# Kernel optimization log

Hardware: AMD Instinct MI355X
Metric: run time of the kernel (lower is better)

## Reference

```python
import jax, jax.numpy as jnp
import numpy as np

NEG_SLOPE = 0.2  # keras 'leaky_relu' default negative slope

def _leaky_relu(t):
    return jnp.where(t >= 0, t, NEG_SLOPE * t)

def setup_inputs() -> dict:
    key = jax.random.key(0)
    kx, kq, kk, kv, ko, kg = jax.random.split(key, 6)
    B, H, W, C, A = 4, 64, 64, 256, 128
    x = jax.random.normal(kx, (B, H, W, C), dtype=jnp.float32)
    # 1x1 conv kernels == [Cin, Cout] matrices; glorot-normal-ish scaling
    Wq = jax.random.normal(kq, (C, A), dtype=jnp.float32) * (2.0 / (C + A)) ** 0.5
    Wk = jax.random.normal(kk, (C, A), dtype=jnp.float32) * (2.0 / (C + A)) ** 0.5
    Wv = jax.random.normal(kv, (C, A), dtype=jnp.float32) * (2.0 / (C + A)) ** 0.5
    Wo = jax.random.normal(ko, (A, C), dtype=jnp.float32) * (2.0 / (A + C)) ** 0.5
    # ChannelLearnableMultiplier weight: truncated_normal(0, 0.01) ~ small values near 0
    w_gamma = jax.random.normal(kg, (1, 1, 1, C), dtype=jnp.float32) * 0.01
    return {"x": x, "Wq": Wq, "Wk": Wk, "Wv": Wv, "Wo": Wo, "w_gamma": w_gamma}

def reference(x, Wq, Wk, Wv, Wo, w_gamma):
    B, H, W, C = x.shape
    A = Wq.shape[1]
    # 1x1 conv projections with leaky_relu activation, flatten spatial -> [B, N, A]
    q = _leaky_relu(jnp.einsum('bhwc,ca->bhwa', x, Wq)).reshape(B, H * W, A)
    k = _leaky_relu(jnp.einsum('bhwc,ca->bhwa', x, Wk)).reshape(B, H * W, A)
    v = _leaky_relu(jnp.einsum('bhwc,ca->bhwa', x, Wv)).reshape(B, H * W, A)
    # keras Attention(use_scale=False, score_mode='dot'): softmax(q k^T) v
    scores = jnp.einsum('bnd,bmd->bnm', q, k)          # [B, N, N]
    attn = jax.nn.softmax(scores, axis=-1)
    o = jnp.einsum('bnm,bmd->bnd', attn, v)            # [B, N, A]
    o = o.reshape(B, H, W, A)
    # output 1x1 conv, linear activation
    y = jnp.einsum('bhwa,ac->bhwc', o, Wo)
    # ChannelLearnableMultiplier: tanh(relu(1 + w)) * y
    return jnp.tanh(jax.nn.relu(1.0 + w_gamma)) * y
```

## Files before the change

### kernel.cpp

```cpp
#include <hip/hip_runtime.h>
#include <hip/hip_bf16.h>
#include <cstdint>
#include <cstddef>

typedef __bf16 bf16x8 __attribute__((ext_vector_type(8)));
typedef _Float16 f16x8 __attribute__((ext_vector_type(8)));
typedef short short8 __attribute__((ext_vector_type(8)));
typedef short short4v __attribute__((ext_vector_type(4)));
typedef float f32x4 __attribute__((ext_vector_type(4)));

__device__ __forceinline__ unsigned short f2bf(float f) {
    union { float f; uint32_t u; } v; v.f = f;
    uint32_t u = v.u;
    return (unsigned short)((u + 0x7FFFu + ((u >> 16) & 1u)) >> 16);
}
__device__ __forceinline__ float bf2f(unsigned short h) {
    union { uint32_t u; float f; } v; v.u = ((uint32_t)h) << 16;
    return v.f;
}
__device__ __forceinline__ unsigned short f2h(float f) {
    union { _Float16 h; unsigned short u; } v; v.h = (_Float16)f;
    return v.u;
}

__global__ __launch_bounds__(256) void prep_kernel(
    const float* __restrict__ Wq, const float* __restrict__ Wk,
    const float* __restrict__ Wv, const float* __restrict__ Wo,
    unsigned short* __restrict__ wt_hi,
    unsigned short* __restrict__ wt_lo,
    unsigned short* __restrict__ wot)
{
    const int bid = blockIdx.x, t = threadIdx.x;
    __shared__ __align__(16) unsigned short Th[128][72], Tl[128][72];
    __shared__ __align__(16) unsigned short T[64][136];
    if (bid < 12) {
        const int proj = bid >> 2, kc = bid & 3;
        const float* W = (proj == 0) ? Wq : ((proj == 1) ? Wk : Wv);
        for (int r = 0; r < 32; ++r) {
            int idx = r * 256 + t;
            int kk = idx >> 7, n = idx & 127;
            float w = W[(size_t)(kc * 64 + kk) * 128 + n];
            unsigned short h = f2bf(w);
            Th[n][kk] = h;
            Tl[n][kk] = f2bf(w - bf2f(h));
        }
        __syncthreads();
        int n = t >> 1, k0 = (t & 1) * 32;
        size_t off = (size_t)proj * 32768 + (size_t)kc * 8192 + (size_t)n * 64 + k0;
        #pragma unroll
        for (int j = 0; j < 4; ++j) {
            *(short8*)(wt_hi + off + j * 8) = *(const short8*)(&Th[n][k0 + j * 8]);
            *(short8*)(wt_lo + off + j * 8) = *(const short8*)(&Tl[n][k0 + j * 8]);
        }
    } else if (bid < 16) {
        const int c0 = (bid - 12) * 64;
        for (int r = 0; r < 32; ++r) {
            int idx = r * 256 + t;
            int a = idx >> 6, cc = idx & 63;
            T[cc][a] = f2bf(Wo[(size_t)a * 256 + c0 + cc]);
        }
        __syncthreads();
        int cc = t >> 2, a0 = (t & 3) * 32;
        #pragma unroll
        for (int j = 0; j < 4; ++j)
            *(short8*)(wot + (size_t)(c0 + cc) * 128 + a0 + j * 8) =
                *(const short8*)(&T[cc][a0 + j * 8]);
    }
}

__global__ __launch_bounds__(256) void qkv_kernel(
    const float* __restrict__ x,
    const unsigned short* __restrict__ wt_hi,
    const unsigned short* __restrict__ wt_lo,
    unsigned short* __restrict__ qkv_ws)
{
    const int rowtile = blockIdx.x;
    const int proj    = blockIdx.y;
    unsigned short* outqk = qkv_ws + (size_t)proj * 2097152u;
    unsigned short* vt    = qkv_ws + (size_t)2 * 2097152u;
    const bool need_lo = (proj < 2);

    const int tid  = threadIdx.x;
    const int lane = tid & 63, wave = tid >> 6;
    const int lo   = lane & 15, quad = lane >> 4;

    __shared__ __align__(16) unsigned short Xh[64][72], Xl[64][72];
    __shared__ __align__(16) unsigned short Wh[128][72], Wl[128][72];

    f32x4 acc[8];
    #pragma unroll
    for (int i = 0; i < 8; ++i) acc[i] = (f32x4){0.f, 0.f, 0.f, 0.f};

    const int wn = tid >> 1, wk0 = (tid & 1) * 32;

    for (int kc = 0; kc < 4; ++kc) {
        __syncthreads();
        #pragma unroll
        for (int i = 0; i < 4; ++i) {
            int flat4 = (i * 256 + tid) * 4;
            int row = flat4 >> 6, col = flat4 & 63;
            float4 tv4 = *(const float4*)(x + (size_t)(rowtile * 64 + row) * 256 + kc * 64 + col);
            float tv[4] = {tv4.x, tv4.y, tv4.z, tv4.w};
            short4v h, l;
            #pragma unroll
            for (int j = 0; j < 4; ++j) {
                unsigned short hj = f2bf(tv[j]);
                h[j] = (short)hj;
                l[j] = (short)f2bf(tv[j] - bf2f(hj));
            }
            *(short4v*)(&Xh[row][col]) = h;
            if (need_lo) *(short4v*)(&Xl[row][col]) = l;
        }
        {
            const size_t off = (size_t)proj * 32768 + (size_t)kc * 8192 + (size_t)wn * 64 + wk0;
            #pragma unroll
            for (int j = 0; j < 4; ++j)
                *(short8*)(&Wh[wn][wk0 + j * 8]) = *(const short8*)(wt_hi + off + j * 8);
            if (need_lo) {
                #pragma unroll
                for (int j = 0; j < 4; ++j)
                    *(short8*)(&Wl[wn][wk0 + j * 8]) = *(const short8*)(wt_lo + off + j * 8);
            }
        }
        __syncthreads();
        #pragma unroll
        for (int ks = 0; ks < 2; ++ks) {
            bf16x8 ah = *(const bf16x8*)(&Xh[wave * 16 + lo][ks * 32 + quad * 8]);
            #pragma unroll
            for (int nb = 0; nb < 8; ++nb) {
                bf16x8 bh = *(const bf16x8*)(&Wh[nb * 16 + lo][ks * 32 + quad * 8]);
                acc[nb] = __builtin_amdgcn_mfma_f32_16x16x32_bf16(ah, bh, acc[nb], 0, 0, 0);
                if (need_lo) {
                    bf16x8 al = *(const bf16x8*)(&Xl[wave * 16 + lo][ks * 32 + quad * 8]);
                    bf16x8 bl = *(const bf16x8*)(&Wl[nb * 16 + lo][ks * 32 + quad * 8]);
                    acc[nb] = __builtin_amdgcn_mfma_f32_16x16x32_bf16(al, bh, acc[nb], 0, 0, 0);
                    acc[nb] = __builtin_amdgcn_mfma_f32_16x16x32_bf16(ah, bl, acc[nb], 0, 0, 0);
                }
            }
        }
    }
    if (proj < 2) {
        #pragma unroll
        for (int nb = 0; nb < 8; ++nb) {
            #pragma unroll
            for (int r = 0; r < 4; ++r) {
                float v = acc[nb][r];
                v = (v >= 0.f) ? v : 0.2f * v;
                int m = rowtile * 64 + wave * 16 + quad * 4 + r;
                outqk[(size_t)m * 128 + nb * 16 + lo] = f2h(v);
            }
        }
    } else {
        const int b  = rowtile >> 6;
        const int sb = (rowtile & 63) * 64;
        #pragma unroll
        for (int nb = 0; nb < 8; ++nb) {
            #pragma unroll
            for (int r = 0; r < 4; ++r) {
                float v = acc[nb][r];
                v = (v >= 0.f) ? v : 0.2f * v;
                int seq = sb + wave * 16 + quad * 4 + r;
                int d   = nb * 16 + lo;
                vt[(size_t)b * 524288 + (size_t)d * 4096 + seq] = f2bf(v);
            }
        }
    }
}

__global__ __launch_bounds__(256) void attn_kernel(
    const unsigned short* __restrict__ qkv_ws,
    unsigned short* __restrict__ part,
    float* __restrict__ lpart,
    int chunk)
{
    const int b  = blockIdx.x;
    const int qt = blockIdx.y;
    const int z  = blockIdx.z;
    const int tid  = threadIdx.x;
    const int lane = tid & 63, wave = tid >> 6;
    const int lo   = lane & 15, quad = lane >> 4;

    const unsigned short* q  = qkv_ws;
    const unsigned short* k  = qkv_ws + 2097152u;
    const unsigned short* vt = qkv_ws + (size_t)2 * 2097152u + (size_t)b * 524288u;

    __shared__ __align__(16) unsigned short Ks[32][136];
    __shared__ __align__(16) unsigned short Vt[128][40];
    __shared__ __align__(16) unsigned short Ps[4][32][40];

    const int qbase = qt * 128 + wave * 32;
    f16x8 qf[2][4];
    #pragma unroll
    for (int g = 0; g < 2; ++g)
        #pragma unroll
        for (int ks = 0; ks < 4; ++ks)
            qf[g][ks] = *(const f16x8*)(q + ((size_t)(b * 4096 + qbase + g * 16 + lo)) * 128
                                          + ks * 32 + quad * 8);

    f32x4 oacc[2][8];
    #pragma unroll
    for (int g = 0; g < 2; ++g)
        #pragma unroll
        for (int i = 0; i < 8; ++i) oacc[g][i] = (f32x4){0.f, 0.f, 0.f, 0.f};
    float lsum[2][4];
    #pragma unroll
    for (int g = 0; g < 2; ++g)
        #pragma unroll
        for (int r = 0; r < 4; ++r) lsum[g][r] = 1e-30f;

    const float LOG2E  = 1.44269504088896f;
    const float NSHIFT = -40.0f * 1.44269504088896f;

    const int c0 = tid, c1 = 256 + tid;
    const int krow0 = c0 >> 4, kcol0 = (c0 & 15) * 8;
    const int krow1 = (c1 - 256) >> 4 + 0;
    const int vd0 = c0 >> 2, vs0 = (c0 & 3) * 8;
    const int vd1 = (c1 - 256) >> 2, vs1 = ((c1 - 256) & 3) * 8;
    const int krow1b = 16 + (tid >> 4), kcol1b = (tid & 15) * 8;
    const int vd1b = 64 + (tid >> 2), vs1b = (tid & 3) * 8;
    (void)krow1; (void)vd1; (void)vs1; (void)c1;

    const int niter = chunk >> 5;
    const int sbase = z * chunk;

    short8 ka, kb, va, vb;
    {
        ka = *(const short8*)(k + ((size_t)(b * 4096 + sbase + krow0)) * 128 + kcol0);
        kb = *(const short8*)(k + ((size_t)(b * 4096 + sbase + krow1b)) * 128 + kcol1b);
        va = *(const short8*)(vt + (size_t)vd0 * 4096 + sbase + vs0);
        vb = *(const short8*)(vt + (size_t)vd1b * 4096 + sbase + vs1b);
    }

    for (int kt = 0; kt < niter; ++kt) {
        __syncthreads();
        *(short8*)(&Ks[krow0][kcol0]) = ka;
        *(short8*)(&Ks[krow1b][kcol1b]) = kb;
        *(short8*)(&Vt[vd0][vs0]) = va;
        *(short8*)(&Vt[vd1b][vs1b]) = vb;
        __syncthreads();
        if (kt + 1 < niter) {
            const int s1 = sbase + (kt + 1) * 32;
            ka = *(const short8*)(k + ((size_t)(b * 4096 + s1 + krow0)) * 128 + kcol0);
            kb = *(const short8*)(k + ((size_t)(b * 4096 + s1 + krow1b)) * 128 + kcol1b);
            va = *(const short8*)(vt + (size_t)vd0 * 4096 + s1 + vs0);
            vb = *(const short8*)(vt + (size_t)vd1b * 4096 + s1 + vs1b);
        }

        f32x4 s[2][2];
        s[0][0] = (f32x4){0.f,0.f,0.f,0.f}; s[0][1] = (f32x4){0.f,0.f,0.f,0.f};
        s[1][0] = (f32x4){0.f,0.f,0.f,0.f}; s[1][1] = (f32x4){0.f,0.f,0.f,0.f};
        #pragma unroll
        for (int ks = 0; ks < 4; ++ks) {
            #pragma unroll
            for (int nb = 0; nb < 2; ++nb) {
                f16x8 bf = *(const f16x8*)(&Ks[nb * 16 + lo][ks * 32 + quad * 8]);
                s[0][nb] = __builtin_amdgcn_mfma_f32_16x16x32_f16(qf[0][ks], bf, s[0][nb], 0, 0, 0);
                s[1][nb] = __builtin_amdgcn_mfma_f32_16x16x32_f16(qf[1][ks], bf, s[1][nb], 0, 0, 0);
            }
        }
        #pragma unroll
        for (int g = 0; g < 2; ++g) {
            #pragma unroll
            for (int nb = 0; nb < 2; ++nb) {
                #pragma unroll
                for (int r = 0; r < 4; ++r) {
                    float t = fminf(fmaf(s[g][nb][r], LOG2E, NSHIFT), 125.0f);
                    union { float f; uint32_t u; } pv; pv.f = exp2f(t);
                    unsigned short pt = (unsigned short)(pv.u >> 16);
                    lsum[g][r] += bf2f(pt);
                    Ps[wave][g * 16 + quad * 4 + r][nb * 16 + lo] = pt;
                }
            }
        }
        bf16x8 pf0 = *(const bf16x8*)(&Ps[wave][lo][quad * 8]);
        bf16x8 pf1 = *(const bf16x8*)(&Ps[wave][16 + lo][quad * 8]);
        #pragma unroll
        for (int nb = 0; nb < 8; ++nb) {
            bf16x8 vf = *(const bf16x8*)(&Vt[nb * 16 + lo][quad * 8]);
            oacc[0][nb] = __builtin_amdgcn_mfma_f32_16x16x32_bf16(pf0, vf, oacc[0][nb], 0, 0, 0);
            oacc[1][nb] = __builtin_amdgcn_mfma_f32_16x16x32_bf16(pf1, vf, oacc[1][nb], 0, 0, 0);
        }
    }

    #pragma unroll
    for (int g = 0; g < 2; ++g) {
        #pragma unroll
        for (int r = 0; r < 4; ++r) {
            float xr = lsum[g][r];
            #pragma unroll
            for (int m = 1; m < 16; m <<= 1) xr += __shfl_xor(xr, m, 64);
            lsum[g][r] = xr;
        }
        #pragma unroll
        for (int nb = 0; nb < 8; ++nb) {
            #pragma unroll
            for (int r = 0; r < 4; ++r) {
                int m = b * 4096 + qbase + g * 16 + quad * 4 + r;
                part[((size_t)z * 16384 + m) * 128 + nb * 16 + lo] = f2bf(oacc[g][nb][r]);
            }
        }
        if (lo == 0) {
            #pragma unroll
            for (int r = 0; r < 4; ++r) {
                int m = b * 4096 + qbase + g * 16 + quad * 4 + r;
                lpart[(size_t)z * 16384 + m] = lsum[g][r];
            }
        }
    }
}

__global__ __launch_bounds__(256) void outproj_kernel(
    const unsigned short* __restrict__ part,
    const float* __restrict__ lpart,
    const unsigned short* __restrict__ wot,
    const float* __restrict__ wg,
    float* __restrict__ out,
    int nsplit)
{
    const int rowtile = blockIdx.x;
    const int ch      = blockIdx.y;
    const int tid  = threadIdx.x;
    const int lane = tid & 63, wave = tid >> 6;
    const int lo   = lane & 15, quad = lane >> 4;

    __shared__ __align__(16) unsigned short Os[64][136];
    __shared__ __align__(16) unsigned short WoT[128][136];

    #pragma unroll
    for (int i = 0; i < 4; ++i) {
        int flat = (i * 256 + tid) * 8;
        int row = flat >> 7, col = flat & 127;
        int m = rowtile * 64 + row;
        float acc8[8] = {0.f,0.f,0.f,0.f,0.f,0.f,0.f,0.f};
        float l = 0.f;
        for (int zz = 0; zz < nsplit; ++zz) {
            short8 t = *(const short8*)(part + ((size_t)zz * 16384 + m) * 128 + col);
            #pragma unroll
            for (int j = 0; j < 8; ++j) acc8[j] += bf2f((unsigned short)t[j]);
            l += lpart[(size_t)zz * 16384 + m];
        }
        float inv = 1.0f / l;
        short8 o8;
        #pragma unroll
        for (int j = 0; j < 8; ++j) o8[j] = (short)f2bf(acc8[j] * inv);
        *(short8*)(&Os[row][col]) = o8;
    }
    {
        int c = tid >> 1, a0 = (tid & 1) * 64;
        #pragma unroll
        for (int j = 0; j < 8; ++j)
            *(short8*)(&WoT[c][a0 + j * 8]) =
                *(const short8*)(wot + (size_t)(ch * 128 + c) * 128 + a0 + j * 8);
    }
    __syncthreads();

    f32x4 acc[8];
    #pragma unroll
    for (int i = 0; i < 8; ++i) acc[i] = (f32x4){0.f, 0.f, 0.f, 0.f};
    #pragma unroll
    for (int ks = 0; ks < 4; ++ks) {
        bf16x8 a = *(const bf16x8*)(&Os[wave * 16 + lo][ks * 32 + quad * 8]);
        #pragma unroll
        for (int nb = 0; nb < 8; ++nb) {
            bf16x8 bf = *(const bf16x8*)(&WoT[nb * 16 + lo][ks * 32 + quad * 8]);
            acc[nb] = __builtin_amdgcn_mfma_f32_16x16x32_bf16(a, bf, acc[nb], 0, 0, 0);
        }
    }
    #pragma unroll
    for (int nb = 0; nb < 8; ++nb) {
        int c = ch * 128 + nb * 16 + lo;
        float g = 1.0f + wg[c];
        if (g < 0.f) g = 0.f;
        g = tanhf(g);
        #pragma unroll
        for (int r = 0; r < 4; ++r) {
            int m = rowtile * 64 + wave * 16 + quad * 4 + r;
            out[(size_t)m * 256 + c] = acc[nb][r] * g;
        }
    }
}

extern "C" void kernel_launch(void* const* d_in, const int* in_sizes, int n_in,
                              void* d_out, int out_size, void* d_ws, size_t ws_size,
                              hipStream_t stream) {
    const float* x  = (const float*)d_in[0];
    const float* Wq = (const float*)d_in[1];
    const float* Wk = (const float*)d_in[2];
    const float* Wv = (const float*)d_in[3];
    const float* Wo = (const float*)d_in[4];
    const float* wg = (const float*)d_in[5];
    float* out = (float*)d_out;

    unsigned short* ws = (unsigned short*)d_ws;
    const int nsplit = (ws_size >= (size_t)47000000) ? 8 : 4;
    const int chunk = 4096 / nsplit;

    unsigned short* qkv_ws = ws;
    unsigned short* part   = ws + (size_t)3 * 2097152u;
    unsigned short* wt_hi  = part;
    unsigned short* wt_lo  = part + 98304u;
    float* lpart = (float*)(part + (size_t)nsplit * 2097152u);
    unsigned short* wot = (unsigned short*)(lpart + (size_t)nsplit * 16384u);

    prep_kernel<<<dim3(16), 256, 0, stream>>>(Wq, Wk, Wv, Wo, wt_hi, wt_lo, wot);
    qkv_kernel<<<dim3(256, 3), 256, 0, stream>>>(x, wt_hi, wt_lo, qkv_ws);
    attn_kernel<<<dim3(4, 32, nsplit), 256, 0, stream>>>(qkv_ws, part, lpart, chunk);
    outproj_kernel<<<dim3(256, 2), 256, 0, stream>>>(part, lpart, wot, wg, out, nsplit);
}
```

Baseline: 178.6 us.

## Precompute x bf16 hi/lo split once and merge outproj channel halves per block

Moves the fp32-to-bf16 hi/lo split of x into the prep kernel, so qkv blocks load ready-made bf16 tiles instead of converting x three times (once per projection). Also precomputes the gamma multiplier once, and has each outproj block loop over both channel halves, so the split-K partial reduction is done once instead of twice. The extra x staging pass adds global traffic and a serial dependency, and outproj now launches half as many blocks.

```diff
diff --git a/kernel.cpp b/kernel.cpp
--- a/kernel.cpp
+++ b/kernel.cpp
@@ -26,13 +26,17 @@
 __global__ __launch_bounds__(256) void prep_kernel(
     const float* __restrict__ Wq, const float* __restrict__ Wk,
     const float* __restrict__ Wv, const float* __restrict__ Wo,
+    const float* __restrict__ wg, const float* __restrict__ x,
     unsigned short* __restrict__ wt_hi,
     unsigned short* __restrict__ wt_lo,
-    unsigned short* __restrict__ wot)
+    unsigned short* __restrict__ wot,
+    float* __restrict__ gamma,
+    unsigned short* __restrict__ xh,
+    unsigned short* __restrict__ xl,
+    int use_pre)
 {
     const int bid = blockIdx.x, t = threadIdx.x;
     __shared__ __align__(16) unsigned short Th[128][72], Tl[128][72];
-    __shared__ __align__(16) unsigned short T[64][136];
     if (bid < 12) {
         const int proj = bid >> 2, kc = bid & 3;
         const float* W = (proj == 0) ? Wq : ((proj == 1) ? Wk : Wv);
@@ -54,25 +58,50 @@
         }
     } else if (bid < 16) {
         const int c0 = (bid - 12) * 64;
+        unsigned short* T = &Th[0][0];
         for (int r = 0; r < 32; ++r) {
             int idx = r * 256 + t;
             int a = idx >> 6, cc = idx & 63;
-            T[cc][a] = f2bf(Wo[(size_t)a * 256 + c0 + cc]);
+            T[cc * 136 + a] = f2bf(Wo[(size_t)a * 256 + c0 + cc]);
         }
         __syncthreads();
         int cc = t >> 2, a0 = (t & 3) * 32;
         #pragma unroll
         for (int j = 0; j < 4; ++j)
             *(short8*)(wot + (size_t)(c0 + cc) * 128 + a0 + j * 8) =
-                *(const short8*)(&T[cc][a0 + j * 8]);
+                *(const short8*)(&T[cc * 136 + a0 + j * 8]);
+    } else if (bid == 16) {
+        float g = 1.0f + wg[t];
+        if (g < 0.f) g = 0.f;
+        gamma[t] = tanhf(g);
+    } else if (use_pre) {
+        const int bx = bid - 17;
+        #pragma unroll 4
+        for (int it = 0; it < 32; ++it) {
+            size_t ci = (size_t)bx * 8192 + it * 256 + t;
+            float4 tv4 = *(const float4*)(x + ci * 4);
+            float tv[4] = {tv4.x, tv4.y, tv4.z, tv4.w};
+            short4v h, l;
+            #pragma unroll
+            for (int j = 0; j < 4; ++j) {
+                unsigned short hj = f2bf(tv[j]);
+                h[j] = (short)hj;
+                l[j] = (short)f2bf(tv[j] - bf2f(hj));
+            }
+            *(short4v*)(xh + ci * 4) = h;
+            *(short4v*)(xl + ci * 4) = l;
+        }
     }
 }
 
 __global__ __launch_bounds__(256) void qkv_kernel(
     const float* __restrict__ x,
+    const unsigned short* __restrict__ xh,
+    const unsigned short* __restrict__ xl,
     const unsigned short* __restrict__ wt_hi,
     const unsigned short* __restrict__ wt_lo,
-    unsigned short* __restrict__ qkv_ws)
+    unsigned short* __restrict__ qkv_ws,
+    int use_pre)
 {
     const int rowtile = blockIdx.x;
     const int proj    = blockIdx.y;
@@ -95,21 +124,32 @@
 
     for (int kc = 0; kc < 4; ++kc) {
         __syncthreads();
-        #pragma unroll
-        for (int i = 0; i < 4; ++i) {
-            int flat4 = (i * 256 + tid) * 4;
-            int row = flat4 >> 6, col = flat4 & 63;
-            float4 tv4 = *(const float4*)(x + (size_t)(rowtile * 64 + row) * 256 + kc * 64 + col);
-            float tv[4] = {tv4.x, tv4.y, tv4.z, tv4.w};
-            short4v h, l;
-            #pragma unroll
-            for (int j = 0; j < 4; ++j) {
-                unsigned short hj = f2bf(tv[j]);
-                h[j] = (short)hj;
-                l[j] = (short)f2bf(tv[j] - bf2f(hj));
-            }
-            *(short4v*)(&Xh[row][col]) = h;
-            if (need_lo) *(short4v*)(&Xl[row][col]) = l;
+        if (use_pre) {
+            #pragma unroll
+            for (int j = 0; j < 2; ++j) {
+                int ci = tid * 2 + j;
+                int row = ci >> 3, col = (ci & 7) * 8;
+                size_t g = (size_t)(rowtile * 64 + row) * 256 + kc * 64 + col;
+                *(short8*)(&Xh[row][col]) = *(const short8*)(xh + g);
+                if (need_lo) *(short8*)(&Xl[row][col]) = *(const short8*)(xl + g);
+            }
+        } else {
+            #pragma unroll
+            for (int i = 0; i < 4; ++i) {
+                int flat4 = (i * 256 + tid) * 4;
+                int row = flat4 >> 6, col = flat4 & 63;
+                float4 tv4 = *(const float4*)(x + (size_t)(rowtile * 64 + row) * 256 + kc * 64 + col);
+                float tv[4] = {tv4.x, tv4.y, tv4.z, tv4.w};
+                short4v h, l;
+                #pragma unroll
+                for (int j = 0; j < 4; ++j) {
+                    unsigned short hj = f2bf(tv[j]);
+                    h[j] = (short)hj;
+                    l[j] = (short)f2bf(tv[j] - bf2f(hj));
+                }
+                *(short4v*)(&Xh[row][col]) = h;
+                if (need_lo) *(short4v*)(&Xl[row][col]) = l;
+            }
         }
         {
             const size_t off = (size_t)proj * 32768 + (size_t)kc * 8192 + (size_t)wn * 64 + wk0;
@@ -211,39 +251,33 @@
     const float LOG2E  = 1.44269504088896f;
     const float NSHIFT = -40.0f * 1.44269504088896f;
 
-    const int c0 = tid, c1 = 256 + tid;
-    const int krow0 = c0 >> 4, kcol0 = (c0 & 15) * 8;
-    const int krow1 = (c1 - 256) >> 4 + 0;
-    const int vd0 = c0 >> 2, vs0 = (c0 & 3) * 8;
-    const int vd1 = (c1 - 256) >> 2, vs1 = ((c1 - 256) & 3) * 8;
-    const int krow1b = 16 + (tid >> 4), kcol1b = (tid & 15) * 8;
-    const int vd1b = 64 + (tid >> 2), vs1b = (tid & 3) * 8;
-    (void)krow1; (void)vd1; (void)vs1; (void)c1;
+    const int krow0 = tid >> 4,        kcol0 = (tid & 15) * 8;
+    const int krow1 = 16 + (tid >> 4), kcol1 = (tid & 15) * 8;
+    const int vd0 = tid >> 2,          vs0 = (tid & 3) * 8;
+    const int vd1 = 64 + (tid >> 2),   vs1 = (tid & 3) * 8;
 
     const int niter = chunk >> 5;
     const int sbase = z * chunk;
 
     short8 ka, kb, va, vb;
-    {
-        ka = *(const short8*)(k + ((size_t)(b * 4096 + sbase + krow0)) * 128 + kcol0);
-        kb = *(const short8*)(k + ((size_t)(b * 4096 + sbase + krow1b)) * 128 + kcol1b);
-        va = *(const short8*)(vt + (size_t)vd0 * 4096 + sbase + vs0);
-        vb = *(const short8*)(vt + (size_t)vd1b * 4096 + sbase + vs1b);
-    }
+    ka = *(const short8*)(k + ((size_t)(b * 4096 + sbase + krow0)) * 128 + kcol0);
+    kb = *(const short8*)(k + ((size_t)(b * 4096 + sbase + krow1)) * 128 + kcol1);
+    va = *(const short8*)(vt + (size_t)vd0 * 4096 + sbase + vs0);
+    vb = *(const short8*)(vt + (size_t)vd1 * 4096 + sbase + vs1);
 
     for (int kt = 0; kt < niter; ++kt) {
         __syncthreads();
         *(short8*)(&Ks[krow0][kcol0]) = ka;
-        *(short8*)(&Ks[krow1b][kcol1b]) = kb;
+        *(short8*)(&Ks[krow1][kcol1]) = kb;
         *(short8*)(&Vt[vd0][vs0]) = va;
-        *(short8*)(&Vt[vd1b][vs1b]) = vb;
+        *(short8*)(&Vt[vd1][vs1]) = vb;
         __syncthreads();
         if (kt + 1 < niter) {
             const int s1 = sbase + (kt + 1) * 32;
             ka = *(const short8*)(k + ((size_t)(b * 4096 + s1 + krow0)) * 128 + kcol0);
-            kb = *(const short8*)(k + ((size_t)(b * 4096 + s1 + krow1b)) * 128 + kcol1b);
+            kb = *(const short8*)(k + ((size_t)(b * 4096 + s1 + krow1)) * 128 + kcol1);
             va = *(const short8*)(vt + (size_t)vd0 * 4096 + s1 + vs0);
-            vb = *(const short8*)(vt + (size_t)vd1b * 4096 + s1 + vs1b);
+            vb = *(const short8*)(vt + (size_t)vd1 * 4096 + s1 + vs1);
         }
 
         f32x4 s[2][2];
@@ -313,12 +347,11 @@
     const unsigned short* __restrict__ part,
     const float* __restrict__ lpart,
     const unsigned short* __restrict__ wot,
-    const float* __restrict__ wg,
+    const float* __restrict__ gamma,
     float* __restrict__ out,
     int nsplit)
 {
     const int rowtile = blockIdx.x;
-    const int ch      = blockIdx.y;
     const int tid  = threadIdx.x;
     const int lane = tid & 63, wave = tid >> 6;
     const int lo   = lane & 15, quad = lane >> 4;
@@ -345,37 +378,37 @@
         for (int j = 0; j < 8; ++j) o8[j] = (short)f2bf(acc8[j] * inv);
         *(short8*)(&Os[row][col]) = o8;
     }
-    {
-        int c = tid >> 1, a0 = (tid & 1) * 64;
+
+    const int wc = tid >> 1, wa0 = (tid & 1) * 64;
+    for (int ch = 0; ch < 2; ++ch) {
+        if (ch) __syncthreads();
         #pragma unroll
         for (int j = 0; j < 8; ++j)
-            *(short8*)(&WoT[c][a0 + j * 8]) =
-                *(const short8*)(wot + (size_t)(ch * 128 + c) * 128 + a0 + j * 8);
-    }
-    __syncthreads();
-
-    f32x4 acc[8];
-    #pragma unroll
-    for (int i = 0; i < 8; ++i) acc[i] = (f32x4){0.f, 0.f, 0.f, 0.f};
-    #pragma unroll
-    for (int ks = 0; ks < 4; ++ks) {
-        bf16x8 a = *(const bf16x8*)(&Os[wave * 16 + lo][ks * 32 + quad * 8]);
+            *(short8*)(&WoT[wc][wa0 + j * 8]) =
+                *(const short8*)(wot + (size_t)(ch * 128 + wc) * 128 + wa0 + j * 8);
+        __syncthreads();
+
+        f32x4 acc[8];
+        #pragma unroll
+        for (int i = 0; i < 8; ++i) acc[i] = (f32x4){0.f, 0.f, 0.f, 0.f};
+        #pragma unroll
+        for (int ks = 0; ks < 4; ++ks) {
+            bf16x8 a = *(const bf16x8*)(&Os[wave * 16 + lo][ks * 32 + quad * 8]);
+            #pragma unroll
+            for (int nb = 0; nb < 8; ++nb) {
+                bf16x8 bf = *(const bf16x8*)(&WoT[nb * 16 + lo][ks * 32 + quad * 8]);
+                acc[nb] = __builtin_amdgcn_mfma_f32_16x16x32_bf16(a, bf, acc[nb], 0, 0, 0);
+            }
+        }
         #pragma unroll
         for (int nb = 0; nb < 8; ++nb) {
-            bf16x8 bf = *(const bf16x8*)(&WoT[nb * 16 + lo][ks * 32 + quad * 8]);
-            acc[nb] = __builtin_amdgcn_mfma_f32_16x16x32_bf16(a, bf, acc[nb], 0, 0, 0);
-        }
-    }
-    #pragma unroll
-    for (int nb = 0; nb < 8; ++nb) {
-        int c = ch * 128 + nb * 16 + lo;
-        float g = 1.0f + wg[c];
-        if (g < 0.f) g = 0.f;
-        g = tanhf(g);
-        #pragma unroll
-        for (int r = 0; r < 4; ++r) {
-            int m = rowtile * 64 + wave * 16 + quad * 4 + r;
-            out[(size_t)m * 256 + c] = acc[nb][r] * g;
+            int c = ch * 128 + nb * 16 + lo;
+            float g = gamma[c];
+            #pragma unroll
+            for (int r = 0; r < 4; ++r) {
+                int m = rowtile * 64 + wave * 16 + quad * 4 + r;
+                out[(size_t)m * 256 + c] = acc[nb][r] * g;
+            }
         }
     }
 }
@@ -392,18 +425,23 @@
     float* out = (float*)d_out;
 
     unsigned short* ws = (unsigned short*)d_ws;
-    const int nsplit = (ws_size >= (size_t)47000000) ? 8 : 4;
-    const int chunk = 4096 / nsplit;
+    const int use_pre = (ws_size >= (size_t)47000000) ? 1 : 0;
+    const int nsplit  = use_pre ? 8 : 4;
+    const int chunk   = 4096 / nsplit;
 
     unsigned short* qkv_ws = ws;
     unsigned short* part   = ws + (size_t)3 * 2097152u;
     unsigned short* wt_hi  = part;
     unsigned short* wt_lo  = part + 98304u;
+    unsigned short* xh     = part + 262144u;
+    unsigned short* xl     = xh + 4194304u;
     float* lpart = (float*)(part + (size_t)nsplit * 2097152u);
     unsigned short* wot = (unsigned short*)(lpart + (size_t)nsplit * 16384u);
-
-    prep_kernel<<<dim3(16), 256, 0, stream>>>(Wq, Wk, Wv, Wo, wt_hi, wt_lo, wot);
-    qkv_kernel<<<dim3(256, 3), 256, 0, stream>>>(x, wt_hi, wt_lo, qkv_ws);
+    float* gamma = (float*)(wot + 32768u);
+
+    prep_kernel<<<dim3(use_pre ? 145 : 17), 256, 0, stream>>>(
+        Wq, Wk, Wv, Wo, wg, x, wt_hi, wt_lo, wot, gamma, xh, xl, use_pre);
+    qkv_kernel<<<dim3(256, 3), 256, 0, stream>>>(x, xh, xl, wt_hi, wt_lo, qkv_ws, use_pre);
     attn_kernel<<<dim3(4, 32, nsplit), 256, 0, stream>>>(qkv_ws, part, lpart, chunk);
-    outproj_kernel<<<dim3(256, 2), 256, 0, stream>>>(part, lpart, wot, wg, out, nsplit);
-}
+    outproj_kernel<<<dim3(256), 256, 0, stream>>>(part, lpart, wot, gamma, out, nsplit);
+}
```

After: 173.9 us. 1.03x faster.

## Double-buffer K/V tiles in attention and merge output-projection channel halves

Applied to the files above, without the earlier changes.

The attention kernel now keeps two LDS buffers for K and V tiles. The next tile is written into the idle buffer after the PV MFMAs, which removes one of the two barriers per iteration, and V is stored in a split layout so each lane reads it contiguously. The output-projection kernel loops over both channel halves inside one block, so the softmax partial combine is no longer done twice. The gamma multiplier is precomputed once in the prep kernel. In exchange, LDS use in attention goes up and the output kernel launches half as many blocks.

```diff
diff --git a/kernel.cpp b/kernel.cpp
--- a/kernel.cpp
+++ b/kernel.cpp
@@ -26,13 +26,14 @@
 __global__ __launch_bounds__(256) void prep_kernel(
     const float* __restrict__ Wq, const float* __restrict__ Wk,
     const float* __restrict__ Wv, const float* __restrict__ Wo,
+    const float* __restrict__ wg,
     unsigned short* __restrict__ wt_hi,
     unsigned short* __restrict__ wt_lo,
-    unsigned short* __restrict__ wot)
+    unsigned short* __restrict__ wot,
+    float* __restrict__ gamma)
 {
     const int bid = blockIdx.x, t = threadIdx.x;
     __shared__ __align__(16) unsigned short Th[128][72], Tl[128][72];
-    __shared__ __align__(16) unsigned short T[64][136];
     if (bid < 12) {
         const int proj = bid >> 2, kc = bid & 3;
         const float* W = (proj == 0) ? Wq : ((proj == 1) ? Wk : Wv);
@@ -54,17 +55,22 @@
         }
     } else if (bid < 16) {
         const int c0 = (bid - 12) * 64;
+        unsigned short* T = &Th[0][0];
         for (int r = 0; r < 32; ++r) {
             int idx = r * 256 + t;
             int a = idx >> 6, cc = idx & 63;
-            T[cc][a] = f2bf(Wo[(size_t)a * 256 + c0 + cc]);
+            T[cc * 136 + a] = f2bf(Wo[(size_t)a * 256 + c0 + cc]);
         }
         __syncthreads();
         int cc = t >> 2, a0 = (t & 3) * 32;
         #pragma unroll
         for (int j = 0; j < 4; ++j)
             *(short8*)(wot + (size_t)(c0 + cc) * 128 + a0 + j * 8) =
-                *(const short8*)(&T[cc][a0 + j * 8]);
+                *(const short8*)(&T[cc * 136 + a0 + j * 8]);
+    } else {
+        float g = 1.0f + wg[t];
+        if (g < 0.f) g = 0.f;
+        gamma[t] = tanhf(g);
     }
 }
 
@@ -184,8 +190,8 @@
     const unsigned short* k  = qkv_ws + 2097152u;
     const unsigned short* vt = qkv_ws + (size_t)2 * 2097152u + (size_t)b * 524288u;
 
-    __shared__ __align__(16) unsigned short Ks[32][136];
-    __shared__ __align__(16) unsigned short Vt[128][40];
+    __shared__ __align__(16) unsigned short Ks[2][32][136];
+    __shared__ __align__(16) unsigned short Vt4[2][4][128][8];
     __shared__ __align__(16) unsigned short Ps[4][32][40];
 
     const int qbase = qt * 128 + wave * 32;
@@ -211,39 +217,33 @@
     const float LOG2E  = 1.44269504088896f;
     const float NSHIFT = -40.0f * 1.44269504088896f;
 
-    const int c0 = tid, c1 = 256 + tid;
-    const int krow0 = c0 >> 4, kcol0 = (c0 & 15) * 8;
-    const int krow1 = (c1 - 256) >> 4 + 0;
-    const int vd0 = c0 >> 2, vs0 = (c0 & 3) * 8;
-    const int vd1 = (c1 - 256) >> 2, vs1 = ((c1 - 256) & 3) * 8;
-    const int krow1b = 16 + (tid >> 4), kcol1b = (tid & 15) * 8;
-    const int vd1b = 64 + (tid >> 2), vs1b = (tid & 3) * 8;
-    (void)krow1; (void)vd1; (void)vs1; (void)c1;
+    const int krow0 = tid >> 4, kcol0 = (tid & 15) * 8;
+    const int krow1 = 16 + (tid >> 4);
+    const int vd = tid >> 2, vc = tid & 3;
 
     const int niter = chunk >> 5;
     const int sbase = z * chunk;
 
     short8 ka, kb, va, vb;
-    {
-        ka = *(const short8*)(k + ((size_t)(b * 4096 + sbase + krow0)) * 128 + kcol0);
-        kb = *(const short8*)(k + ((size_t)(b * 4096 + sbase + krow1b)) * 128 + kcol1b);
-        va = *(const short8*)(vt + (size_t)vd0 * 4096 + sbase + vs0);
-        vb = *(const short8*)(vt + (size_t)vd1b * 4096 + sbase + vs1b);
-    }
+    ka = *(const short8*)(k + ((size_t)(b * 4096 + sbase + krow0)) * 128 + kcol0);
+    kb = *(const short8*)(k + ((size_t)(b * 4096 + sbase + krow1)) * 128 + kcol0);
+    va = *(const short8*)(vt + (size_t)vd * 4096 + sbase + vc * 8);
+    vb = *(const short8*)(vt + (size_t)(vd + 64) * 4096 + sbase + vc * 8);
+    *(short8*)(&Ks[0][krow0][kcol0]) = ka;
+    *(short8*)(&Ks[0][krow1][kcol0]) = kb;
+    *(short8*)(&Vt4[0][vc][vd][0]) = va;
+    *(short8*)(&Vt4[0][vc][vd + 64][0]) = vb;
+    __syncthreads();
 
     for (int kt = 0; kt < niter; ++kt) {
-        __syncthreads();
-        *(short8*)(&Ks[krow0][kcol0]) = ka;
-        *(short8*)(&Ks[krow1b][kcol1b]) = kb;
-        *(short8*)(&Vt[vd0][vs0]) = va;
-        *(short8*)(&Vt[vd1b][vs1b]) = vb;
-        __syncthreads();
-        if (kt + 1 < niter) {
+        const int cur = kt & 1, nxt = cur ^ 1;
+        const bool more = (kt + 1 < niter);
+        if (more) {
             const int s1 = sbase + (kt + 1) * 32;
             ka = *(const short8*)(k + ((size_t)(b * 4096 + s1 + krow0)) * 128 + kcol0);
-            kb = *(const short8*)(k + ((size_t)(b * 4096 + s1 + krow1b)) * 128 + kcol1b);
-            va = *(const short8*)(vt + (size_t)vd0 * 4096 + s1 + vs0);
-            vb = *(const short8*)(vt + (size_t)vd1b * 4096 + s1 + vs1b);
+            kb = *(const short8*)(k + ((size_t)(b * 4096 + s1 + krow1)) * 128 + kcol0);
+            va = *(const short8*)(vt + (size_t)vd * 4096 + s1 + vc * 8);
+            vb = *(const short8*)(vt + (size_t)(vd + 64) * 4096 + s1 + vc * 8);
         }
 
         f32x4 s[2][2];
@@ -253,7 +253,7 @@
         for (int ks = 0; ks < 4; ++ks) {
             #pragma unroll
             for (int nb = 0; nb < 2; ++nb) {
-                f16x8 bf = *(const f16x8*)(&Ks[nb * 16 + lo][ks * 32 + quad * 8]);
+                f16x8 bf = *(const f16x8*)(&Ks[cur][nb * 16 + lo][ks * 32 + quad * 8]);
                 s[0][nb] = __builtin_amdgcn_mfma_f32_16x16x32_f16(qf[0][ks], bf, s[0][nb], 0, 0, 0);
                 s[1][nb] = __builtin_amdgcn_mfma_f32_16x16x32_f16(qf[1][ks], bf, s[1][nb], 0, 0, 0);
             }
@@ -276,10 +276,17 @@
         bf16x8 pf1 = *(const bf16x8*)(&Ps[wave][16 + lo][quad * 8]);
         #pragma unroll
         for (int nb = 0; nb < 8; ++nb) {
-            bf16x8 vf = *(const bf16x8*)(&Vt[nb * 16 + lo][quad * 8]);
+            bf16x8 vf = *(const bf16x8*)(&Vt4[cur][quad][nb * 16 + lo][0]);
             oacc[0][nb] = __builtin_amdgcn_mfma_f32_16x16x32_bf16(pf0, vf, oacc[0][nb], 0, 0, 0);
             oacc[1][nb] = __builtin_amdgcn_mfma_f32_16x16x32_bf16(pf1, vf, oacc[1][nb], 0, 0, 0);
         }
+        if (more) {
+            *(short8*)(&Ks[nxt][krow0][kcol0]) = ka;
+            *(short8*)(&Ks[nxt][krow1][kcol0]) = kb;
+            *(short8*)(&Vt4[nxt][vc][vd][0]) = va;
+            *(short8*)(&Vt4[nxt][vc][vd + 64][0]) = vb;
+        }
+        __syncthreads();
     }
 
     #pragma unroll
@@ -313,12 +320,11 @@
     const unsigned short* __restrict__ part,
     const float* __restrict__ lpart,
     const unsigned short* __restrict__ wot,
-    const float* __restrict__ wg,
+    const float* __restrict__ gamma,
     float* __restrict__ out,
     int nsplit)
 {
     const int rowtile = blockIdx.x;
-    const int ch      = blockIdx.y;
     const int tid  = threadIdx.x;
     const int lane = tid & 63, wave = tid >> 6;
     const int lo   = lane & 15, quad = lane >> 4;
@@ -345,37 +351,37 @@
         for (int j = 0; j < 8; ++j) o8[j] = (short)f2bf(acc8[j] * inv);
         *(short8*)(&Os[row][col]) = o8;
     }
-    {
-        int c = tid >> 1, a0 = (tid & 1) * 64;
+
+    const int wc = tid >> 1, wa0 = (tid & 1) * 64;
+    for (int ch = 0; ch < 2; ++ch) {
+        if (ch) __syncthreads();
         #pragma unroll
         for (int j = 0; j < 8; ++j)
-            *(short8*)(&WoT[c][a0 + j * 8]) =
-                *(const short8*)(wot + (size_t)(ch * 128 + c) * 128 + a0 + j * 8);
-    }
-    __syncthreads();
-
-    f32x4 acc[8];
-    #pragma unroll
-    for (int i = 0; i < 8; ++i) acc[i] = (f32x4){0.f, 0.f, 0.f, 0.f};
-    #pragma unroll
-    for (int ks = 0; ks < 4; ++ks) {
-        bf16x8 a = *(const bf16x8*)(&Os[wave * 16 + lo][ks * 32 + quad * 8]);
+            *(short8*)(&WoT[wc][wa0 + j * 8]) =
+                *(const short8*)(wot + (size_t)(ch * 128 + wc) * 128 + wa0 + j * 8);
+        __syncthreads();
+
+        f32x4 acc[8];
+        #pragma unroll
+        for (int i = 0; i < 8; ++i) acc[i] = (f32x4){0.f, 0.f, 0.f, 0.f};
+        #pragma unroll
+        for (int ks = 0; ks < 4; ++ks) {
+            bf16x8 a = *(const bf16x8*)(&Os[wave * 16 + lo][ks * 32 + quad * 8]);
+            #pragma unroll
+            for (int nb = 0; nb < 8; ++nb) {
+                bf16x8 bf = *(const bf16x8*)(&WoT[nb * 16 + lo][ks * 32 + quad * 8]);
+                acc[nb] = __builtin_amdgcn_mfma_f32_16x16x32_bf16(a, bf, acc[nb], 0, 0, 0);
+            }
+        }
         #pragma unroll
         for (int nb = 0; nb < 8; ++nb) {
-            bf16x8 bf = *(const bf16x8*)(&WoT[nb * 16 + lo][ks * 32 + quad * 8]);
-            acc[nb] = __builtin_amdgcn_mfma_f32_16x16x32_bf16(a, bf, acc[nb], 0, 0, 0);
-        }
-    }
-    #pragma unroll
-    for (int nb = 0; nb < 8; ++nb) {
-        int c = ch * 128 + nb * 16 + lo;
-        float g = 1.0f + wg[c];
-        if (g < 0.f) g = 0.f;
-        g = tanhf(g);
-        #pragma unroll
-        for (int r = 0; r < 4; ++r) {
-            int m = rowtile * 64 + wave * 16 + quad * 4 + r;
-            out[(size_t)m * 256 + c] = acc[nb][r] * g;
+            int c = ch * 128 + nb * 16 + lo;
+            float g = gamma[c];
+            #pragma unroll
+            for (int r = 0; r < 4; ++r) {
+                int m = rowtile * 64 + wave * 16 + quad * 4 + r;
+                out[(size_t)m * 256 + c] = acc[nb][r] * g;
+            }
         }
     }
 }
@@ -393,7 +399,7 @@
 
     unsigned short* ws = (unsigned short*)d_ws;
     const int nsplit = (ws_size >= (size_t)47000000) ? 8 : 4;
-    const int chunk = 4096 / nsplit;
+    const int chunk  = 4096 / nsplit;
 
     unsigned short* qkv_ws = ws;
     unsigned short* part   = ws + (size_t)3 * 2097152u;
@@ -401,9 +407,10 @@
     unsigned short* wt_lo  = part + 98304u;
     float* lpart = (float*)(part + (size_t)nsplit * 2097152u);
     unsigned short* wot = (unsigned short*)(lpart + (size_t)nsplit * 16384u);
-
-    prep_kernel<<<dim3(16), 256, 0, stream>>>(Wq, Wk, Wv, Wo, wt_hi, wt_lo, wot);
+    float* gamma = (float*)(wot + 32768u);
+
+    prep_kernel<<<dim3(17), 256, 0, stream>>>(Wq, Wk, Wv, Wo, wg, wt_hi, wt_lo, wot, gamma);
     qkv_kernel<<<dim3(256, 3), 256, 0, stream>>>(x, wt_hi, wt_lo, qkv_ws);
     attn_kernel<<<dim3(4, 32, nsplit), 256, 0, stream>>>(qkv_ws, part, lpart, chunk);
-    outproj_kernel<<<dim3(256, 2), 256, 0, stream>>>(part, lpart, wot, wg, out, nsplit);
-}
+    outproj_kernel<<<dim3(256), 256, 0, stream>>>(part, lpart, wot, gamma, out, nsplit);
+}
```

Result: no change. 181.3 us (+1.5%).
